# Kernel optimization log

Measured on AMD Instinct MI355X. Metric: run time of the kernel, lower is better.

The kernel has to match this reference:

```python
import jax, jax.numpy as jnp
import numpy as np

NEG_SLOPE = 0.1

def leaky(x):
    return jnp.where(x >= 0, x, NEG_SLOPE * x)

def setup_inputs() -> dict:
    key = jax.random.key(0)
    ks = jax.random.split(key, 12)
    B, C, H, W, K, COUT = 2, 64, 160, 224, 16, 64
    HW = H * W
    xyz = jax.random.normal(ks[0], (B, 3, H, W), jnp.float32)
    features = jax.random.normal(ks[1], (B, C, H, W), jnp.float32)
    sampled_xyz = jax.random.normal(ks[2], (B, 3, H, W), jnp.float32)
    knn_indices = jax.random.randint(ks[3], (B, HW, K), 0, HW, dtype=jnp.int32).astype(jnp.int64)
    valid_knn_mask = jax.random.randint(ks[4], (B, HW, K), 0, 2, dtype=jnp.int32).astype(bool)
    # weight_net: MLP2d(3, [8, 16]) -> two 1x1 convs (pointwise linears)
    w1 = jax.random.normal(ks[5], (8, 3), jnp.float32) * 0.3
    b1 = jax.random.normal(ks[6], (8,), jnp.float32) * 0.01
    w2 = jax.random.normal(ks[7], (16, 8), jnp.float32) * 0.2
    b2 = jax.random.normal(ks[8], (16,), jnp.float32) * 0.01
    # final linear: 16*(C+3) -> COUT
    fan_in = 16 * (C + 3)
    w_lin = jax.random.normal(ks[9], (COUT, fan_in), jnp.float32) / np.sqrt(fan_in)
    b_lin = jax.random.normal(ks[10], (COUT,), jnp.float32) * 0.01
    return {"xyz": xyz, "features": features, "sampled_xyz": sampled_xyz,
            "knn_indices": knn_indices, "valid_knn_mask": valid_knn_mask,
            "w1": w1, "b1": b1, "w2": w2, "b2": b2, "w_lin": w_lin, "b_lin": b_lin}

def reference(xyz, features, sampled_xyz, knn_indices, valid_knn_mask,
              w1, b1, w2, b2, w_lin, b_lin):
    B, C, H, W = features.shape
    h, w = sampled_xyz.shape[2:]
    N = h * w          # number of query points
    K = knn_indices.shape[2]
    HW = H * W
    mask = valid_knn_mask[..., None].astype(xyz.dtype)          # [B,N,K,1]
    idx = knn_indices.reshape(B, N * K, 1)                      # gather index
    # channel-last source features: [xyz ; features] -> [B,HW,C+3]
    feats_cl = jnp.concatenate([xyz, features], axis=1).reshape(B, C + 3, HW).transpose(0, 2, 1)
    knn_feats = jnp.take_along_axis(feats_cl, idx, axis=1).reshape(B, N, K, C + 3) * mask
    # neighbor coordinates, masked: [B,N,K,3]
    xyz_cl = xyz.reshape(B, 3, HW).transpose(0, 2, 1)
    knn_xyz = jnp.take_along_axis(xyz_cl, idx, axis=1).reshape(B, N, K, 3) * mask
    new_xyz = sampled_xyz.reshape(B, 3, N).transpose(0, 2, 1)   # [B,N,3]
    rel = knn_xyz - new_xyz[:, :, None, :]                      # [B,N,K,3]
    # weight_net: 1x1 conv MLP 3 -> 8 -> 16 with leaky_relu(0.1)
    h1 = leaky(jnp.einsum('bnkc,oc->bnko', rel, w1) + b1)       # [B,N,K,8]
    weights = leaky(jnp.einsum('bnkc,oc->bnko', h1, w2) + b2)   # [B,N,K,16]
    # weighted aggregation over the K neighbors: [B,N,16,C+3]
    agg = jnp.einsum('bnkf,bnkc->bnfc', weights, knn_feats)
    agg = agg.reshape(B, N, 16 * (C + 3))
    out = jnp.einsum('bnf,of->bno', agg, w_lin) + b_lin         # [B,N,COUT]
    out = leaky(out)                                            # norm = Identity
    return out.transpose(0, 2, 1).reshape(B, -1, h, w)
```

## Files before the change

kernel.cpp:

```cpp
#include <hip/hip_runtime.h>
#include <hip/hip_bf16.h>

#define HWv   35840
#define NPTS  35840
#define Bv    2
#define Kv    16
#define CP3   67
#define COUT  64
#define PPB   16
#define NBLK_PER_B (NPTS / PPB)
#define KDIM  1088
#define ASTR  1096
#define WTSTR 264

typedef __attribute__((ext_vector_type(4))) float  f32x4;
typedef __attribute__((ext_vector_type(8))) short  bf16x8;

static __device__ __forceinline__ unsigned short f2bf(float f) {
    unsigned int u = __float_as_uint(f);
    unsigned int r = (u + 0x7FFFu + ((u >> 16) & 1u)) >> 16;
    return (unsigned short)r;
}
static __device__ __forceinline__ float leaky(float v) { return v >= 0.f ? v : 0.1f * v; }

__global__ __launch_bounds__(256) void transpose_kernel(const float* __restrict__ xyz,
                                                        const float* __restrict__ feat,
                                                        unsigned short* __restrict__ feats_bf,
                                                        float* __restrict__ xyz_cl) {
    __shared__ float tile[68][65];
    int t = threadIdx.x;
    int blk = blockIdx.x;
    int b = blk / 560;
    int hw0 = (blk % 560) * 64;
    int j = t & 63, cq = t >> 6;
    for (int cc = 0; cc < 17; ++cc) {
        int c = cc * 4 + cq;
        float v = 0.f;
        if (c < 64)      v = feat[((long)b * 64 + c) * HWv + hw0 + j];
        else if (c < 67) v = xyz[((long)b * 3 + (c - 64)) * HWv + hw0 + j];
        tile[c][j] = v;
    }
    __syncthreads();
    int r = t >> 2, q = t & 3;
    unsigned short* dst = feats_bf + ((long)b * HWv + hw0 + r) * 64;
    #pragma unroll
    for (int i = q; i < 16; i += 4) {
        ushort4 v;
        v.x = f2bf(tile[i * 4 + 0][r]); v.y = f2bf(tile[i * 4 + 1][r]);
        v.z = f2bf(tile[i * 4 + 2][r]); v.w = f2bf(tile[i * 4 + 3][r]);
        *(ushort4*)(dst + i * 4) = v;
    }
    if (q == 0) {
        float4 x4 = make_float4(tile[64][r], tile[65][r], tile[66][r], 0.f);
        *(float4*)(xyz_cl + ((long)b * HWv + hw0 + r) * 4) = x4;
    }
}

__global__ __launch_bounds__(256) void wl_bf16_kernel(const float* __restrict__ w_lin,
                                                      unsigned short* __restrict__ wl_bf) {
    int e = blockIdx.x * 256 + threadIdx.x;
    if (e >= COUT * KDIM) return;
    int o  = e / KDIM;
    int fc = e - o * KDIM;
    int f  = fc / 68;
    int c  = fc - f * 68;
    float v = 0.f;
    if (c < 64)      v = w_lin[o * (16 * CP3) + f * CP3 + 3 + c];
    else if (c < 67) v = w_lin[o * (16 * CP3) + f * CP3 + (c - 64)];
    wl_bf[e] = f2bf(v);
}

__global__ __launch_bounds__(256, 4) void pointconv_main(
        const unsigned short* __restrict__ feats_bf,
        const float*  __restrict__ xyz_cl,
        const unsigned short* __restrict__ wl_bf,
        const int*    __restrict__ knn_idx,
        const int*    __restrict__ mask,
        const float*  __restrict__ sampled,
        const float*  __restrict__ w1,
        const float*  __restrict__ b1,
        const float*  __restrict__ w2,
        const float*  __restrict__ b2,
        const float*  __restrict__ b_lin,
        float*        __restrict__ out) {
    __shared__ __align__(16) char sBuf[PPB * ASTR * 2];
    __shared__ int   sRow[PPB][Kv];
    __shared__ float sMask[PPB][Kv];
    __shared__ float sNx[PPB][4];
    __shared__ float sNet[240];

    float* sXyz = (float*)sBuf;
    float* sWt  = (float*)(sBuf + 3072);
    unsigned short* sAgg = (unsigned short*)sBuf;

    int t = threadIdx.x;
    int blk = blockIdx.x;
    int b = blk / NBLK_PER_B;
    int n0 = (blk % NBLK_PER_B) * PPB;
    int p = t >> 4, u = t & 15;

    {
        int base = (b * NPTS + n0 + p) * Kv + u;
        int g = knn_idx[base];
        float mf = mask[base] ? 1.f : 0.f;
        int row = b * HWv + g;
        sRow[p][u]  = row * 128;
        sMask[p][u] = mf;
        float4 x4 = *(const float4*)(xyz_cl + (long)row * 4);
        float* xd = sXyz + (p * Kv + u) * 3;
        xd[0] = x4.x * mf; xd[1] = x4.y * mf; xd[2] = x4.z * mf;
        if (t < 240) {
            float v;
            if (t < 24)       v = w1[t];
            else if (t < 32)  v = b1[t - 24];
            else if (t < 160) v = w2[t - 32];
            else if (t < 176) v = b2[t - 160];
            else              v = b_lin[t - 176];
            sNet[t] = v;
        }
        if (t < PPB * 3) { int pp = t / 3, c = t - pp * 3; sNx[pp][c] = sampled[(b * 3 + c) * HWv + n0 + pp]; }
    }
    __syncthreads();

    const char* fb = (const char*)feats_bf;
    ushort4 pre[8];
    #pragma unroll
    for (int k = 0; k < 8; ++k) pre[k] = *(const ushort4*)(fb + sRow[p][k] + u * 8);

    {
        int k = u;
        const float* W1 = sNet;
        const float* B1 = sNet + 24;
        const float* W2 = sNet + 32;
        const float* B2 = sNet + 160;
        const float* xs = sXyz + (p * Kv + k) * 3;
        float r0 = xs[0] - sNx[p][0];
        float r1 = xs[1] - sNx[p][1];
        float r2 = xs[2] - sNx[p][2];
        float mf = sMask[p][k];
        float h[8];
        #pragma unroll
        for (int i = 0; i < 8; ++i)
            h[i] = leaky(W1[i * 3] * r0 + W1[i * 3 + 1] * r1 + W1[i * 3 + 2] * r2 + B1[i]);
        float wk[16];
        #pragma unroll
        for (int f = 0; f < 16; ++f) {
            float v = B2[f];
            #pragma unroll
            for (int i = 0; i < 8; ++i) v += W2[f * 8 + i] * h[i];
            wk[f] = leaky(v) * mf;
        }
        f32x4* wdst = (f32x4*)(sWt + p * WTSTR + k * 16);
        wdst[0] = (f32x4){wk[0], wk[1], wk[2], wk[3]};
        wdst[1] = (f32x4){wk[4], wk[5], wk[6], wk[7]};
        wdst[2] = (f32x4){wk[8], wk[9], wk[10], wk[11]};
        wdst[3] = (f32x4){wk[12], wk[13], wk[14], wk[15]};
    }
    __syncthreads();

    f32x4 agg4[16];
    #pragma unroll
    for (int f = 0; f < 16; ++f) agg4[f] = (f32x4){0.f, 0.f, 0.f, 0.f};
    float ax = 0.f, ay = 0.f, az = 0.f;

    #pragma unroll
    for (int k = 0; k < Kv; ++k) {
        ushort4 hv = pre[k & 7];
        if (k < 8) pre[k & 7] = *(const ushort4*)(fb + sRow[p][k + 8] + u * 8);
        unsigned int dlo = ((unsigned int)hv.y << 16) | hv.x;
        unsigned int dhi = ((unsigned int)hv.w << 16) | hv.z;
        f32x4 fv4;
        fv4[0] = __uint_as_float(dlo << 16);
        fv4[1] = __uint_as_float(dlo & 0xffff0000u);
        fv4[2] = __uint_as_float(dhi << 16);
        fv4[3] = __uint_as_float(dhi & 0xffff0000u);
        const f32x4* wt4 = (const f32x4*)(sWt + p * WTSTR + k * 16);
        f32x4 w0 = wt4[0], w1v = wt4[1], w2v = wt4[2], w3v = wt4[3];
        agg4[0]  += fv4 * w0[0];  agg4[1]  += fv4 * w0[1];
        agg4[2]  += fv4 * w0[2];  agg4[3]  += fv4 * w0[3];
        agg4[4]  += fv4 * w1v[0]; agg4[5]  += fv4 * w1v[1];
        agg4[6]  += fv4 * w1v[2]; agg4[7]  += fv4 * w1v[3];
        agg4[8]  += fv4 * w2v[0]; agg4[9]  += fv4 * w2v[1];
        agg4[10] += fv4 * w2v[2]; agg4[11] += fv4 * w2v[3];
        agg4[12] += fv4 * w3v[0]; agg4[13] += fv4 * w3v[1];
        agg4[14] += fv4 * w3v[2]; agg4[15] += fv4 * w3v[3];
        float wtv = sWt[p * WTSTR + k * 16 + u];
        const float* xs = sXyz + (p * Kv + k) * 3;
        ax += wtv * xs[0]; ay += wtv * xs[1]; az += wtv * xs[2];
    }
    __syncthreads();

    {
        #pragma unroll
        for (int f = 0; f < 16; ++f) {
            ushort4 hv;
            hv.x = f2bf(agg4[f][0]); hv.y = f2bf(agg4[f][1]);
            hv.z = f2bf(agg4[f][2]); hv.w = f2bf(agg4[f][3]);
            *(ushort4*)&sAgg[p * ASTR + f * 68 + u * 4] = hv;
        }
        ushort4 hx;
        hx.x = f2bf(ax); hx.y = f2bf(ay); hx.z = f2bf(az); hx.w = 0;
        *(ushort4*)&sAgg[p * ASTR + u * 68 + 64] = hx;
    }
    __syncthreads();

    {
        int w = t >> 6, l = t & 63;
        int row  = l & 15;
        int kgrp = l >> 4;
        const bf16x8* aptr = (const bf16x8*)&sAgg[row * ASTR + kgrp * 8];
        const bf16x8* bptr = (const bf16x8*)(wl_bf + (w * 16 + row) * KDIM + kgrp * 8);
        f32x4 acc0 = {0.f, 0.f, 0.f, 0.f}, acc1 = {0.f, 0.f, 0.f, 0.f};
        #pragma unroll
        for (int kt = 0; kt < 17; ++kt)
            acc0 = __builtin_amdgcn_mfma_f32_16x16x32_bf16(aptr[kt * 4], bptr[kt * 4], acc0, 0, 0, 0);
        #pragma unroll
        for (int kt = 17; kt < 34; ++kt)
            acc1 = __builtin_amdgcn_mfma_f32_16x16x32_bf16(aptr[kt * 4], bptr[kt * 4], acc1, 0, 0, 0);
        f32x4 acc = acc0 + acc1;
        int o = w * 16 + row;
        float bias = sNet[176 + o];
        float4 res;
        res.x = leaky(acc[0] + bias);
        res.y = leaky(acc[1] + bias);
        res.z = leaky(acc[2] + bias);
        res.w = leaky(acc[3] + bias);
        *(float4*)(out + (long)(b * COUT + o) * HWv + n0 + kgrp * 4) = res;
    }
}

extern "C" void kernel_launch(void* const* d_in, const int* in_sizes, int n_in,
                              void* d_out, int out_size, void* d_ws, size_t ws_size,
                              hipStream_t stream) {
    const float* xyz      = (const float*)d_in[0];
    const float* features = (const float*)d_in[1];
    const float* sampled  = (const float*)d_in[2];
    const int*   knn_idx  = (const int*)  d_in[3];
    const int*   mask     = (const int*)  d_in[4];
    const float* w1       = (const float*)d_in[5];
    const float* b1       = (const float*)d_in[6];
    const float* w2       = (const float*)d_in[7];
    const float* b2       = (const float*)d_in[8];
    const float* w_lin    = (const float*)d_in[9];
    const float* b_lin    = (const float*)d_in[10];
    float* out = (float*)d_out;

    unsigned short* feats_bf = (unsigned short*)d_ws;
    float* xyz_cl = (float*)((char*)d_ws + (size_t)Bv * HWv * 64 * 2);
    unsigned short* wl_bf = (unsigned short*)((char*)xyz_cl + (size_t)Bv * HWv * 4 * 4);

    transpose_kernel<<<Bv * 560, 256, 0, stream>>>(xyz, features, feats_bf, xyz_cl);
    wl_bf16_kernel<<<(COUT * KDIM + 255) / 256, 256, 0, stream>>>(w_lin, wl_bf);
    pointconv_main<<<Bv * NBLK_PER_B, 256, 0, stream>>>(feats_bf, xyz_cl, wl_bf, knn_idx, mask,
                                                        sampled, w1, b1, w2, b2, b_lin, out);
}
```

Baseline: 127.9 us.

## Replace block barriers with wave-local syncs and per-wave shared-memory setup

Each wave now loads its own copy of the MLP weights and its own query coordinates into shared memory, so the first two block-wide barriers can become wave-local barriers plus an LDS waitcnt. The mask and relative coordinates stay in registers instead of going through shared memory. The explicit 8-deep feature prefetch before the weight-net computation is dropped in favour of plain loads inside the aggregation loop. This removes cross-wave stalls but loses the early gather prefetch that hid global-memory latency behind the MLP, and it adds redundant writes of the same weights from every wave.

```diff
diff --git a/kernel.cpp b/kernel.cpp
--- a/kernel.cpp
+++ b/kernel.cpp
@@ -15,6 +15,13 @@
 
 typedef __attribute__((ext_vector_type(4))) float  f32x4;
 typedef __attribute__((ext_vector_type(8))) short  bf16x8;
+
+#define WAVE_SYNC() do {                                        \
+    __builtin_amdgcn_wave_barrier();                            \
+    asm volatile("s_waitcnt lgkmcnt(0)" ::: "memory");          \
+    __builtin_amdgcn_sched_barrier(0);                          \
+    __builtin_amdgcn_wave_barrier();                            \
+} while (0)
 
 static __device__ __forceinline__ unsigned short f2bf(float f) {
     unsigned int u = __float_as_uint(f);
@@ -85,7 +92,6 @@
         float*        __restrict__ out) {
     __shared__ __align__(16) char sBuf[PPB * ASTR * 2];
     __shared__ int   sRow[PPB][Kv];
-    __shared__ float sMask[PPB][Kv];
     __shared__ float sNx[PPB][4];
     __shared__ float sNet[240];
 
@@ -98,46 +104,46 @@
     int b = blk / NBLK_PER_B;
     int n0 = (blk % NBLK_PER_B) * PPB;
     int p = t >> 4, u = t & 15;
-
-    {
-        int base = (b * NPTS + n0 + p) * Kv + u;
-        int g = knn_idx[base];
-        float mf = mask[base] ? 1.f : 0.f;
-        int row = b * HWv + g;
-        sRow[p][u]  = row * 128;
-        sMask[p][u] = mf;
-        float4 x4 = *(const float4*)(xyz_cl + (long)row * 4);
-        float* xd = sXyz + (p * Kv + u) * 3;
-        xd[0] = x4.x * mf; xd[1] = x4.y * mf; xd[2] = x4.z * mf;
-        if (t < 240) {
+    int w = t >> 6, l = t & 63;
+
+    int base = (b * NPTS + n0 + p) * Kv + u;
+    int g = knn_idx[base];
+    float mf = mask[base] ? 1.f : 0.f;
+    int row = b * HWv + g;
+    sRow[p][u] = row * 128;
+    float4 x4 = *(const float4*)(xyz_cl + (long)row * 4);
+    float xd0 = x4.x * mf, xd1 = x4.y * mf, xd2 = x4.z * mf;
+    {
+        float* xs = sXyz + (p * Kv + u) * 3;
+        xs[0] = xd0; xs[1] = xd1; xs[2] = xd2;
+    }
+    #pragma unroll
+    for (int i0 = 0; i0 < 4; ++i0) {
+        int i = i0 * 64 + l;
+        if (i < 240) {
             float v;
-            if (t < 24)       v = w1[t];
-            else if (t < 32)  v = b1[t - 24];
-            else if (t < 160) v = w2[t - 32];
-            else if (t < 176) v = b2[t - 160];
-            else              v = b_lin[t - 176];
-            sNet[t] = v;
+            if (i < 24)       v = w1[i];
+            else if (i < 32)  v = b1[i - 24];
+            else if (i < 160) v = w2[i - 32];
+            else if (i < 176) v = b2[i - 160];
+            else              v = b_lin[i - 176];
+            sNet[i] = v;
         }
-        if (t < PPB * 3) { int pp = t / 3, c = t - pp * 3; sNx[pp][c] = sampled[(b * 3 + c) * HWv + n0 + pp]; }
-    }
-    __syncthreads();
-
-    const char* fb = (const char*)feats_bf;
-    ushort4 pre[8];
-    #pragma unroll
-    for (int k = 0; k < 8; ++k) pre[k] = *(const ushort4*)(fb + sRow[p][k] + u * 8);
-
-    {
-        int k = u;
+    }
+    if (l < 12) {
+        int pp = (w << 2) + (l / 3), c = l - (l / 3) * 3;
+        sNx[pp][c] = sampled[(b * 3 + c) * HWv + n0 + pp];
+    }
+    WAVE_SYNC();
+
+    {
         const float* W1 = sNet;
         const float* B1 = sNet + 24;
         const float* W2 = sNet + 32;
         const float* B2 = sNet + 160;
-        const float* xs = sXyz + (p * Kv + k) * 3;
-        float r0 = xs[0] - sNx[p][0];
-        float r1 = xs[1] - sNx[p][1];
-        float r2 = xs[2] - sNx[p][2];
-        float mf = sMask[p][k];
+        float r0 = xd0 - sNx[p][0];
+        float r1 = xd1 - sNx[p][1];
+        float r2 = xd2 - sNx[p][2];
         float h[8];
         #pragma unroll
         for (int i = 0; i < 8; ++i)
@@ -150,30 +156,28 @@
             for (int i = 0; i < 8; ++i) v += W2[f * 8 + i] * h[i];
             wk[f] = leaky(v) * mf;
         }
-        f32x4* wdst = (f32x4*)(sWt + p * WTSTR + k * 16);
+        f32x4* wdst = (f32x4*)(sWt + p * WTSTR + u * 16);
         wdst[0] = (f32x4){wk[0], wk[1], wk[2], wk[3]};
         wdst[1] = (f32x4){wk[4], wk[5], wk[6], wk[7]};
         wdst[2] = (f32x4){wk[8], wk[9], wk[10], wk[11]};
         wdst[3] = (f32x4){wk[12], wk[13], wk[14], wk[15]};
     }
-    __syncthreads();
+    WAVE_SYNC();
 
     f32x4 agg4[16];
     #pragma unroll
     for (int f = 0; f < 16; ++f) agg4[f] = (f32x4){0.f, 0.f, 0.f, 0.f};
     float ax = 0.f, ay = 0.f, az = 0.f;
 
+    const char* fb = (const char*)feats_bf;
     #pragma unroll
     for (int k = 0; k < Kv; ++k) {
-        ushort4 hv = pre[k & 7];
-        if (k < 8) pre[k & 7] = *(const ushort4*)(fb + sRow[p][k + 8] + u * 8);
-        unsigned int dlo = ((unsigned int)hv.y << 16) | hv.x;
-        unsigned int dhi = ((unsigned int)hv.w << 16) | hv.z;
+        uint2 hv = *(const uint2*)(fb + sRow[p][k] + u * 8);
         f32x4 fv4;
-        fv4[0] = __uint_as_float(dlo << 16);
-        fv4[1] = __uint_as_float(dlo & 0xffff0000u);
-        fv4[2] = __uint_as_float(dhi << 16);
-        fv4[3] = __uint_as_float(dhi & 0xffff0000u);
+        fv4[0] = __uint_as_float(hv.x << 16);
+        fv4[1] = __uint_as_float(hv.x & 0xffff0000u);
+        fv4[2] = __uint_as_float(hv.y << 16);
+        fv4[3] = __uint_as_float(hv.y & 0xffff0000u);
         const f32x4* wt4 = (const f32x4*)(sWt + p * WTSTR + k * 16);
         f32x4 w0 = wt4[0], w1v = wt4[1], w2v = wt4[2], w3v = wt4[3];
         agg4[0]  += fv4 * w0[0];  agg4[1]  += fv4 * w0[1];
@@ -205,11 +209,10 @@
     __syncthreads();
 
     {
-        int w = t >> 6, l = t & 63;
-        int row  = l & 15;
-        int kgrp = l >> 4;
-        const bf16x8* aptr = (const bf16x8*)&sAgg[row * ASTR + kgrp * 8];
-        const bf16x8* bptr = (const bf16x8*)(wl_bf + (w * 16 + row) * KDIM + kgrp * 8);
+        int row16 = l & 15;
+        int kgrp  = l >> 4;
+        const bf16x8* aptr = (const bf16x8*)&sAgg[row16 * ASTR + kgrp * 8];
+        const bf16x8* bptr = (const bf16x8*)(wl_bf + (w * 16 + row16) * KDIM + kgrp * 8);
         f32x4 acc0 = {0.f, 0.f, 0.f, 0.f}, acc1 = {0.f, 0.f, 0.f, 0.f};
         #pragma unroll
         for (int kt = 0; kt < 17; ++kt)
@@ -218,7 +221,7 @@
         for (int kt = 17; kt < 34; ++kt)
             acc1 = __builtin_amdgcn_mfma_f32_16x16x32_bf16(aptr[kt * 4], bptr[kt * 4], acc1, 0, 0, 0);
         f32x4 acc = acc0 + acc1;
-        int o = w * 16 + row;
+        int o = w * 16 + row16;
         float bias = sNet[176 + o];
         float4 res;
         res.x = leaky(acc[0] + bias);
```

Result: slower. 152.2 us (+19.0%).
